# Kernel optimization log

Measured on AMD Instinct MI355X. Metric: run time of the kernel, lower is better.

The kernel has to match this reference:

```python
import jax, jax.numpy as jnp
import numpy as np
import math

N_HEAD = 16
K_SPARSE = 64

def setup_inputs() -> dict:
    key = jax.random.key(0)
    ks = jax.random.split(key, 12)
    B, T, C = 1, 2048, 1024
    s = 0.02
    return {
        "x":   jax.random.normal(ks[0], (B, T, C), jnp.float32),
        "Wq":  jax.random.normal(ks[1], (C, C), jnp.float32) * s,
        "bq":  jax.random.normal(ks[2], (C,), jnp.float32) * s,
        "Wk":  jax.random.normal(ks[3], (C, C), jnp.float32) * s,
        "bk":  jax.random.normal(ks[4], (C,), jnp.float32) * s,
        "Wv":  jax.random.normal(ks[5], (C, C), jnp.float32) * s,
        "bv":  jax.random.normal(ks[6], (C,), jnp.float32) * s,
        "Wo":  jax.random.normal(ks[7], (C, C), jnp.float32) * s,
        "bo":  jax.random.normal(ks[8], (C,), jnp.float32) * s,
        "Wks": jax.random.normal(ks[9], (C,), jnp.float32) * s,
        "bks": jax.random.normal(ks[10], (), jnp.float32) * s,
    }

def reference(x, Wq, bq, Wk, bk, Wv, bv, Wo, bo, Wks, bks):
    B, T, C = x.shape
    nh = N_HEAD
    hs = C // nh
    k_val = min(K_SPARSE, T)

    # projections -> (B, nh, T, hs)   (torch Linear: x @ W.T + b)
    q = (x @ Wq.T + bq).reshape(B, T, nh, hs).transpose(0, 2, 1, 3)
    k = (x @ Wk.T + bk).reshape(B, T, nh, hs).transpose(0, 2, 1, 3)
    v = (x @ Wv.T + bv).reshape(B, T, nh, hs).transpose(0, 2, 1, 3)

    # key scorer: per-token scalar score (B, T)
    key_scores = x @ Wks + bks

    # causal masking of scores, then per-query top-k key selection
    pos = jnp.arange(T)
    causal = pos[None, :] <= pos[:, None]                      # (T, T), True where key<=query
    masked = jnp.where(causal[None], key_scores[:, None, :], -jnp.inf)  # (B, T, T)
    _, top_k_idx = jax.lax.top_k(masked, k_val)                # (B, T, k)
    top_k_idx = jnp.minimum(top_k_idx, pos[None, :, None])     # clamp to <= query pos

    # gather sparse keys/values: (B, nh, T, k, hs)
    bi = jnp.arange(B)[:, None, None, None]
    hi = jnp.arange(nh)[None, :, None, None]
    gi = top_k_idx[:, None, :, :]                              # (B, 1, T, k)
    sparse_k = k[bi, hi, gi]                                   # (B, nh, T, k, hs)
    sparse_v = v[bi, hi, gi]

    scale = 1.0 / math.sqrt(hs)
    logits = jnp.einsum('bhtd,bhtkd->bhtk', q, sparse_k) * scale
    probs = jax.nn.softmax(logits, axis=-1)
    out = jnp.einsum('bhtk,bhtkd->bhtd', probs, sparse_v)      # (B, nh, T, hs)
    out = out.transpose(0, 2, 1, 3).reshape(B, T, C)
    return out @ Wo.T + bo
```

## Files before the change

### kernel.cpp

```cpp
#include <hip/hip_runtime.h>
#include <hip/hip_bf16.h>
#include <cstdint>
#include <cstddef>

#define T_DIM 2048
#define C_DIM 1024
#define NH 16
#define HS 64
#define KSP 64

#define GBM 128
#define GBN 64
#define GBK 128
#define OBM 64
#define OBN 64

#define ATB 32
#define USLOT 96
#define KSTR 72

typedef short short8 __attribute__((ext_vector_type(8)));
typedef float f32x4 __attribute__((ext_vector_type(4)));
typedef _Float16 half2_t __attribute__((ext_vector_type(2)));

__device__ __forceinline__ float bfu2f(unsigned short u) {
  unsigned v = ((unsigned)u) << 16;
  return __builtin_bit_cast(float, v);
}
__device__ __forceinline__ unsigned short f2bfu(float f) {
  unsigned u = __builtin_bit_cast(unsigned, f);
  unsigned r = (u + 0x7fffu + ((u >> 16) & 1u)) >> 16;
  return (unsigned short)r;
}
__device__ __forceinline__ unsigned short f2h(float f) {
  _Float16 h = (_Float16)f;
  return __builtin_bit_cast(unsigned short, h);
}
__device__ __forceinline__ float bflo(unsigned u) {
  return __builtin_bit_cast(float, u << 16);
}
__device__ __forceinline__ float bfhi(unsigned u) {
  return __builtin_bit_cast(float, u & 0xffff0000u);
}

__device__ __forceinline__ float dot2h(unsigned kbits, unsigned qbits, float acc) {
#if __has_builtin(__builtin_amdgcn_fdot2)
  return __builtin_amdgcn_fdot2(__builtin_bit_cast(half2_t, kbits),
                                __builtin_bit_cast(half2_t, qbits), acc, false);
#else
  half2_t kk = __builtin_bit_cast(half2_t, kbits);
  half2_t qq = __builtin_bit_cast(half2_t, qbits);
  return acc + (float)kk.x * (float)qq.x + (float)kk.y * (float)qq.y;
#endif
}

#define GLOAD_LDS16(gp, lp)                                                  \
  __builtin_amdgcn_global_load_lds(                                          \
      (const __attribute__((address_space(1))) void*)(gp),                   \
      (__attribute__((address_space(3))) void*)(lp), 16, 0, 0)

#define NSCORE (T_DIM / 4)
#define NCONV ((T_DIM * C_DIM + 4 * C_DIM * C_DIM) / 4 / 256)
__global__ __launch_bounds__(256) void convert_scores_kernel(
    const float* __restrict__ x, const float* __restrict__ Wq,
    const float* __restrict__ Wk, const float* __restrict__ Wv,
    const float* __restrict__ Wo, const float* __restrict__ Wks,
    const float* __restrict__ bks,
    unsigned short* __restrict__ xb, unsigned short* __restrict__ Wqb,
    unsigned short* __restrict__ Wkb, unsigned short* __restrict__ Wvb,
    unsigned short* __restrict__ Wob, float* __restrict__ scores) {
  if (blockIdx.x < NSCORE) {
    const int t = blockIdx.x * 4 + (threadIdx.x >> 6);
    const int lane = threadIdx.x & 63;
    const float* xrow = x + (size_t)t * C_DIM;
    float acc = 0.f;
    #pragma unroll 4
    for (int i = lane; i < C_DIM; i += 64)
      acc += xrow[i] * Wks[i];
    #pragma unroll
    for (int o = 32; o; o >>= 1) acc += __shfl_xor(acc, o);
    if (lane == 0) scores[t] = acc + bks[0];
    return;
  }
  const int i = (blockIdx.x - NSCORE) * 256 + threadIdx.x;
  const int NX4 = T_DIM * C_DIM / 4;
  const int NW4 = C_DIM * C_DIM / 4;
  const float* src;
  unsigned short* dst;
  int j = i;
  if (j < NX4) { src = x; dst = xb; }
  else {
    j -= NX4;
    int w = j / NW4;
    j -= w * NW4;
    src = (w == 0) ? Wq : (w == 1) ? Wk : (w == 2) ? Wv : Wo;
    dst = (w == 0) ? Wqb : (w == 1) ? Wkb : (w == 2) ? Wvb : Wob;
  }
  float4 f = reinterpret_cast<const float4*>(src)[j];
  ushort4 o;
  o.x = f2bfu(f.x); o.y = f2bfu(f.y); o.z = f2bfu(f.z); o.w = f2bfu(f.w);
  reinterpret_cast<ushort4*>(dst)[j] = o;
}

__device__ __forceinline__ void gemm_body_128x64(
    const unsigned short* __restrict__ A, const unsigned short* __restrict__ W,
    f32x4 acc[4][2], int bm, int bn, int tid,
    unsigned short* As, unsigned short* Ws) {
  const int w = tid >> 6, lane = tid & 63;
  const int quad = lane >> 4, r = lane & 15;
  const int wm = (w >> 1) * 64, wn = (w & 1) * 32;
  const int sub = lane >> 4;
  const int c = lane & 15;
  const unsigned short* Arow[8];
  const unsigned short* Wrow[4];
  #pragma unroll
  for (int i = 0; i < 8; ++i) {
    const int row = w * 32 + i * 4 + sub;
    Arow[i] = A + (size_t)(bm * GBM + row) * C_DIM + ((c ^ (row & 7)) * 8);
  }
  #pragma unroll
  for (int i = 0; i < 4; ++i) {
    const int row = w * 16 + i * 4 + sub;
    Wrow[i] = W + (size_t)(bn * GBN + row) * C_DIM + ((c ^ (row & 7)) * 8);
  }
  for (int kb = 0; kb < C_DIM; kb += GBK) {
    #pragma unroll
    for (int i = 0; i < 8; ++i)
      GLOAD_LDS16(Arow[i] + kb, &As[(w * 32 + i * 4) * GBK]);
    #pragma unroll
    for (int i = 0; i < 4; ++i)
      GLOAD_LDS16(Wrow[i] + kb, &Ws[(w * 16 + i * 4) * GBK]);
    __syncthreads();
    #pragma unroll
    for (int ks = 0; ks < 4; ++ks) {
      const int pc = ((ks * 4 + quad) ^ (r & 7)) * 8;
      short8 af[4], bfr[2];
      #pragma unroll
      for (int mi = 0; mi < 4; ++mi)
        af[mi] = *reinterpret_cast<const short8*>(&As[(wm + mi * 16 + r) * GBK + pc]);
      #pragma unroll
      for (int ni = 0; ni < 2; ++ni)
        bfr[ni] = *reinterpret_cast<const short8*>(&Ws[(wn + ni * 16 + r) * GBK + pc]);
      #pragma unroll
      for (int mi = 0; mi < 4; ++mi)
        #pragma unroll
        for (int ni = 0; ni < 2; ++ni)
          acc[mi][ni] = __builtin_amdgcn_mfma_f32_16x16x32_bf16(af[mi], bfr[ni], acc[mi][ni], 0, 0, 0);
    }
    __syncthreads();
  }
}

#define NRANK (T_DIM / 4)
__global__ __launch_bounds__(256) void gemm_qkv_rank_kernel(
    const unsigned short* __restrict__ A,
    const unsigned short* __restrict__ Wq, const unsigned short* __restrict__ Wk,
    const unsigned short* __restrict__ Wv,
    const float* __restrict__ bq, const float* __restrict__ bk,
    const float* __restrict__ bv,
    unsigned short* __restrict__ qo, unsigned short* __restrict__ ko,
    unsigned short* __restrict__ vo,
    const float* __restrict__ scores, int* __restrict__ sorted_idx) {
  __shared__ unsigned short lds[(GBM + GBN) * GBK];
  const int tid = threadIdx.x;
  if (blockIdx.x < NRANK) {
    float* ss = reinterpret_cast<float*>(lds);
    for (int j = tid; j < T_DIM; j += 256) ss[j] = scores[j];
    __syncthreads();
    const int w = tid >> 6, lane = tid & 63;
    const int i = blockIdx.x * 4 + w;
    const float si = ss[i];
    int rank = 0;
    #pragma unroll
    for (int step = 0; step < T_DIM / 64; ++step) {
      const int j = step * 64 + lane;
      const float sj = ss[j];
      rank += (int)((sj > si) || (sj == si && j < i));
    }
    #pragma unroll
    for (int o = 32; o; o >>= 1) rank += __shfl_xor(rank, o);
    if (lane == 0) sorted_idx[rank] = i;
    return;
  }
  const int bid = blockIdx.x - NRANK;
  const int per = (T_DIM / GBM) * (C_DIM / GBN);
  const int which = bid / per;
  const int rem = bid % per;
  const int bm = rem / (C_DIM / GBN);
  const int bn = rem % (C_DIM / GBN);
  const unsigned short* W = (which == 0) ? Wq : (which == 1) ? Wk : Wv;
  const float* bias = (which == 0) ? bq : (which == 1) ? bk : bv;
  unsigned short* out = (which == 0) ? qo : (which == 1) ? ko : vo;
  f32x4 acc[4][2] = {};
  gemm_body_128x64(A, W, acc, bm, bn, tid, lds, lds + GBM * GBK);
  const int w = tid >> 6, lane = tid & 63;
  const int quad = lane >> 4, r = lane & 15;
  const int wm = (w >> 1) * 64, wn = (w & 1) * 32;
  #pragma unroll
  for (int mi = 0; mi < 4; ++mi) {
    #pragma unroll
    for (int ni = 0; ni < 2; ++ni) {
      const int col = bn * GBN + wn + ni * 16 + r;
      const float bf = bias[col];
      #pragma unroll
      for (int i = 0; i < 4; ++i) {
        const int row = bm * GBM + wm + mi * 16 + quad * 4 + i;
        const float val = acc[mi][ni][i] + bf;
        out[(size_t)row * C_DIM + col] = (which == 2) ? f2bfu(val) : f2h(val);
      }
    }
  }
}

__device__ __forceinline__ void gemm_body_64x64(
    const unsigned short* __restrict__ A, const unsigned short* __restrict__ W,
    f32x4 acc[2][2], int bm, int bn, int tid) {
  __shared__ unsigned short As[OBM * GBK];
  __shared__ unsigned short Ws[OBN * GBK];
  const int w = tid >> 6, lane = tid & 63;
  const int quad = lane >> 4, r = lane & 15;
  const int wm = (w >> 1) * 32, wn = (w & 1) * 32;
  const int sub = lane >> 4;
  const int c = lane & 15;
  const unsigned short* Arow[4];
  const unsigned short* Wrow[4];
  #pragma unroll
  for (int i = 0; i < 4; ++i) {
    const int row = w * 16 + i * 4 + sub;
    Arow[i] = A + (size_t)(bm * OBM + row) * C_DIM + ((c ^ (row & 7)) * 8);
    Wrow[i] = W + (size_t)(bn * OBN + row) * C_DIM + ((c ^ (row & 7)) * 8);
  }
  for (int kb = 0; kb < C_DIM; kb += GBK) {
    #pragma unroll
    for (int i = 0; i < 4; ++i)
      GLOAD_LDS16(Arow[i] + kb, &As[(w * 16 + i * 4) * GBK]);
    #pragma unroll
    for (int i = 0; i < 4; ++i)
      GLOAD_LDS16(Wrow[i] + kb, &Ws[(w * 16 + i * 4) * GBK]);
    __syncthreads();
    #pragma unroll
    for (int ks = 0; ks < 4; ++ks) {
      const int pc = ((ks * 4 + quad) ^ (r & 7)) * 8;
      short8 af[2], bfr[2];
      #pragma unroll
      for (int mi = 0; mi < 2; ++mi)
        af[mi] = *reinterpret_cast<const short8*>(&As[(wm + mi * 16 + r) * GBK + pc]);
      #pragma unroll
      for (int ni = 0; ni < 2; ++ni)
        bfr[ni] = *reinterpret_cast<const short8*>(&Ws[(wn + ni * 16 + r) * GBK + pc]);
      #pragma unroll
      for (int mi = 0; mi < 2; ++mi)
        #pragma unroll
        for (int ni = 0; ni < 2; ++ni)
          acc[mi][ni] = __builtin_amdgcn_mfma_f32_16x16x32_bf16(af[mi], bfr[ni], acc[mi][ni], 0, 0, 0);
    }
    __syncthreads();
  }
}

__global__ __launch_bounds__(256) void gemm_o_f32_kernel(
    const unsigned short* __restrict__ A, const unsigned short* __restrict__ W,
    const float* __restrict__ bias, float* __restrict__ out) {
  const int tid = threadIdx.x;
  const int bm = blockIdx.x / (C_DIM / OBN);
  const int bn = blockIdx.x % (C_DIM / OBN);
  f32x4 acc[2][2] = {};
  gemm_body_64x64(A, W, acc, bm, bn, tid);
  const int w = tid >> 6, lane = tid & 63;
  const int quad = lane >> 4, r = lane & 15;
  const int wm = (w >> 1) * 32, wn = (w & 1) * 32;
  #pragma unroll
  for (int mi = 0; mi < 2; ++mi) {
    #pragma unroll
    for (int ni = 0; ni < 2; ++ni) {
      const int col = bn * OBN + wn + ni * 16 + r;
      const float bf = bias[col];
      #pragma unroll
      for (int i = 0; i < 4; ++i) {
        const int row = bm * OBM + wm + mi * 16 + quad * 4 + i;
        out[(size_t)row * C_DIM + col] = acc[mi][ni][i] + bf;
      }
    }
  }
}

__global__ __launch_bounds__(256) void select_kernel(
    const int* __restrict__ sorted_idx, int* __restrict__ sel) {
  const int tid = threadIdx.x;
  const int w = tid >> 6, lane = tid & 63;
  const int t = blockIdx.x * 4 + w;
  int* dst = sel + (size_t)t * KSP;
  if (t <= 63) {
    dst[lane] = (lane < t) ? lane : t;
    return;
  }
  const unsigned long long lt_mask = (1ull << lane) - 1ull;
  int count = 0;
  for (int chunk = 0; chunk < T_DIM / 64 && count < KSP; ++chunk) {
    int s = sorted_idx[chunk * 64 + lane];
    s = (s < 0) ? 0 : (s > T_DIM - 1 ? T_DIM - 1 : s);
    const bool ok = (s <= t);
    const unsigned long long mm = __ballot(ok);
    const int pos = count + __popcll(mm & lt_mask);
    if (ok && pos < KSP) dst[pos] = s;
    count += __popcll(mm);
  }
}

__global__ __launch_bounds__(256) void attn_kernel(
    const unsigned short* __restrict__ q, const unsigned short* __restrict__ k,
    const unsigned short* __restrict__ v, const int* __restrict__ sel,
    unsigned short* __restrict__ attn_out) {
  __shared__ unsigned short Kl[USLOT * KSTR];
  __shared__ unsigned short Vl[USLOT * KSTR];
  __shared__ short map_s[T_DIM];
  __shared__ short slots_tab[ATB][KSP];
  __shared__ short urows[USLOT];
  __shared__ int Ucnt;
  const int tb = blockIdx.x >> 4;
  const int h = blockIdx.x & (NH - 1);
  const int t0 = tb * ATB;
  const int tid = threadIdx.x;
  const int w = tid >> 6, lane = tid & 63;
  #pragma unroll
  for (int i = 0; i < T_DIM / 256; ++i) map_s[tid + i * 256] = -1;
  __syncthreads();
  int rowreg[ATB * KSP / 256];
  #pragma unroll
  for (int i = 0; i < ATB * KSP / 256; ++i) {
    rowreg[i] = sel[(size_t)t0 * KSP + tid + i * 256];
    map_s[rowreg[i]] = 1;
  }
  __syncthreads();
  if (w == 0) {
    const unsigned long long lt_mask = (1ull << lane) - 1ull;
    int count = 0;
    const int nch = (t0 + ATB + 63) >> 6;
    for (int c = 0; c < nch; ++c) {
      const int rowi = c * 64 + lane;
      const bool ok = (map_s[rowi] == 1);
      const unsigned long long mm = __ballot(ok);
      const int pos = count + __popcll(mm & lt_mask);
      if (ok) { map_s[rowi] = (short)pos; urows[pos] = (short)rowi; }
      count += __popcll(mm);
    }
    if (lane == 0) Ucnt = count;
  }
  __syncthreads();
  #pragma unroll
  for (int i = 0; i < ATB * KSP / 256; ++i)
    (&slots_tab[0][0])[tid + i * 256] = map_s[rowreg[i]];
  {
    const int U = Ucnt;
    const int e8 = tid & 7;
    for (int s = tid >> 3; s < U; s += 32) {
      const int row = urows[s];
      const size_t gb = (size_t)row * C_DIM + h * HS + e8 * 8;
      *reinterpret_cast<uint4*>(&Kl[s * KSTR + e8 * 8]) =
          *reinterpret_cast<const uint4*>(k + gb);
      *reinterpret_cast<uint4*>(&Vl[s * KSTR + e8 * 8]) =
          *reinterpret_cast<const uint4*>(v + gb);
    }
  }
  __syncthreads();
  const int c8 = lane & 7;
  const int ksub = lane >> 3;
  for (int i = 0; i < ATB / 4; ++i) {
    const int tt = w * (ATB / 4) + i;
    const int t = t0 + tt;
    const uint4 qraw =
        *reinterpret_cast<const uint4*>(q + (size_t)t * C_DIM + h * HS + 8 * c8);
    int slot[8];
    #pragma unroll
    for (int jj = 0; jj < 8; ++jj) slot[jj] = slots_tab[tt][8 * jj + ksub];
    float l[8];
    #pragma unroll
    for (int jj = 0; jj < 8; ++jj) {
      const uint4 raw =
          *reinterpret_cast<const uint4*>(&Kl[slot[jj] * KSTR + 8 * c8]);
      float pl = dot2h(raw.x, qraw.x, 0.f);
      pl = dot2h(raw.y, qraw.y, pl);
      pl = dot2h(raw.z, qraw.z, pl);
      pl = dot2h(raw.w, qraw.w, pl);
      pl *= 0.125f;
      pl += __shfl_xor(pl, 1);
      pl += __shfl_xor(pl, 2);
      pl += __shfl_xor(pl, 4);
      l[jj] = pl;
    }
    float m = l[0];
    #pragma unroll
    for (int jj = 1; jj < 8; ++jj) m = fmaxf(m, l[jj]);
    m = fmaxf(m, __shfl_xor(m, 8));
    m = fmaxf(m, __shfl_xor(m, 16));
    m = fmaxf(m, __shfl_xor(m, 32));
    float sum = 0.f;
    #pragma unroll
    for (int jj = 0; jj < 8; ++jj) {
      l[jj] = __expf(l[jj] - m);
      sum += l[jj];
    }
    sum += __shfl_xor(sum, 8);
    sum += __shfl_xor(sum, 16);
    sum += __shfl_xor(sum, 32);
    const float rs = 1.0f / sum;
    float a[8] = {0.f, 0.f, 0.f, 0.f, 0.f, 0.f, 0.f, 0.f};
    #pragma unroll
    for (int jj = 0; jj < 8; ++jj) {
      const uint4 raw =
          *reinterpret_cast<const uint4*>(&Vl[slot[jj] * KSTR + 8 * c8]);
      const float p = l[jj] * rs;
      a[0] += p * bflo(raw.x); a[1] += p * bfhi(raw.x);
      a[2] += p * bflo(raw.y); a[3] += p * bfhi(raw.y);
      a[4] += p * bflo(raw.z); a[5] += p * bfhi(raw.z);
      a[6] += p * bflo(raw.w); a[7] += p * bfhi(raw.w);
    }
    #pragma unroll
    for (int o = 8; o <= 32; o <<= 1) {
      #pragma unroll
      for (int z = 0; z < 8; ++z) a[z] += __shfl_xor(a[z], o);
    }
    if (ksub == 0) {
      ushort4 o0, o1;
      o0.x = f2bfu(a[0]); o0.y = f2bfu(a[1]); o0.z = f2bfu(a[2]); o0.w = f2bfu(a[3]);
      o1.x = f2bfu(a[4]); o1.y = f2bfu(a[5]); o1.z = f2bfu(a[6]); o1.w = f2bfu(a[7]);
      ushort4* dst =
          reinterpret_cast<ushort4*>(attn_out + (size_t)t * C_DIM + h * HS + 8 * c8);
      dst[0] = o0;
      dst[1] = o1;
    }
  }
}

extern "C" void kernel_launch(void* const* d_in, const int* in_sizes, int n_in,
                              void* d_out, int out_size, void* d_ws, size_t ws_size,
                              hipStream_t stream) {
  const float* x   = (const float*)d_in[0];
  const float* Wq  = (const float*)d_in[1];
  const float* bq  = (const float*)d_in[2];
  const float* Wk  = (const float*)d_in[3];
  const float* bk  = (const float*)d_in[4];
  const float* Wv  = (const float*)d_in[5];
  const float* bv  = (const float*)d_in[6];
  const float* Wo  = (const float*)d_in[7];
  const float* bo  = (const float*)d_in[8];
  const float* Wks = (const float*)d_in[9];
  const float* bks = (const float*)d_in[10];
  float* out = (float*)d_out;

  char* ws = (char*)d_ws;
  size_t off = 0;
  float* scores = (float*)(ws + off); off += 8192;
  int*   sorted = (int*)(ws + off);   off += 8192;
  int*   sel    = (int*)(ws + off);   off += (size_t)T_DIM * KSP * 4;
  unsigned short* xb  = (unsigned short*)(ws + off); off += (size_t)T_DIM * C_DIM * 2;
  unsigned short* Wqb = (unsigned short*)(ws + off); off += (size_t)C_DIM * C_DIM * 2;
  unsigned short* Wkb = (unsigned short*)(ws + off); off += (size_t)C_DIM * C_DIM * 2;
  unsigned short* Wvb = (unsigned short*)(ws + off); off += (size_t)C_DIM * C_DIM * 2;
  unsigned short* Wob = (unsigned short*)(ws + off); off += (size_t)C_DIM * C_DIM * 2;
  unsigned short* qb  = (unsigned short*)(ws + off); off += (size_t)T_DIM * C_DIM * 2;
  unsigned short* kb  = (unsigned short*)(ws + off); off += (size_t)T_DIM * C_DIM * 2;
  unsigned short* vb  = (unsigned short*)(ws + off); off += (size_t)T_DIM * C_DIM * 2;
  unsigned short* ab  = xb;

  convert_scores_kernel<<<NSCORE + NCONV, 256, 0, stream>>>(
      x, Wq, Wk, Wv, Wo, Wks, bks, xb, Wqb, Wkb, Wvb, Wob, scores);

  gemm_qkv_rank_kernel<<<NRANK + 3 * (T_DIM / GBM) * (C_DIM / GBN), 256, 0,
                         stream>>>(
      xb, Wqb, Wkb, Wvb, bq, bk, bv, qb, kb, vb, scores, sorted);

  select_kernel<<<T_DIM / 4, 256, 0, stream>>>(sorted, sel);

  attn_kernel<<<(T_DIM / ATB) * NH, 256, 0, stream>>>(qb, kb, vb, sel, ab);

  gemm_o_f32_kernel<<<(T_DIM / OBM) * (C_DIM / OBN), 256, 0, stream>>>(
      ab, Wob, bo, out);
}
```

Before: 170.8 us.

## Fuse top-k selection into attention and build per-block union from first query

New measurement: 160.9 us. 5.8% less time.

```diff
diff --git a/kernel.cpp b/kernel.cpp
--- a/kernel.cpp
+++ b/kernel.cpp
@@ -15,18 +15,14 @@
 #define OBM 64
 #define OBN 64
 
-#define ATB 32
-#define USLOT 96
-#define KSTR 72
+#define ATB 16
+#define USLOT (KSP + ATB - 1)
+#define KSTR 66
 
 typedef short short8 __attribute__((ext_vector_type(8)));
 typedef float f32x4 __attribute__((ext_vector_type(4)));
 typedef _Float16 half2_t __attribute__((ext_vector_type(2)));
 
-__device__ __forceinline__ float bfu2f(unsigned short u) {
-  unsigned v = ((unsigned)u) << 16;
-  return __builtin_bit_cast(float, v);
-}
 __device__ __forceinline__ unsigned short f2bfu(float f) {
   unsigned u = __builtin_bit_cast(unsigned, f);
   unsigned r = (u + 0x7fffu + ((u >> 16) & 1u)) >> 16;
@@ -284,76 +280,60 @@
   }
 }
 
-__global__ __launch_bounds__(256) void select_kernel(
-    const int* __restrict__ sorted_idx, int* __restrict__ sel) {
-  const int tid = threadIdx.x;
-  const int w = tid >> 6, lane = tid & 63;
-  const int t = blockIdx.x * 4 + w;
-  int* dst = sel + (size_t)t * KSP;
-  if (t <= 63) {
-    dst[lane] = (lane < t) ? lane : t;
-    return;
-  }
-  const unsigned long long lt_mask = (1ull << lane) - 1ull;
-  int count = 0;
-  for (int chunk = 0; chunk < T_DIM / 64 && count < KSP; ++chunk) {
-    int s = sorted_idx[chunk * 64 + lane];
-    s = (s < 0) ? 0 : (s > T_DIM - 1 ? T_DIM - 1 : s);
-    const bool ok = (s <= t);
-    const unsigned long long mm = __ballot(ok);
-    const int pos = count + __popcll(mm & lt_mask);
-    if (ok && pos < KSP) dst[pos] = s;
-    count += __popcll(mm);
-  }
-}
-
 __global__ __launch_bounds__(256) void attn_kernel(
     const unsigned short* __restrict__ q, const unsigned short* __restrict__ k,
-    const unsigned short* __restrict__ v, const int* __restrict__ sel,
+    const unsigned short* __restrict__ v, const int* __restrict__ sorted_idx,
     unsigned short* __restrict__ attn_out) {
   __shared__ unsigned short Kl[USLOT * KSTR];
   __shared__ unsigned short Vl[USLOT * KSTR];
   __shared__ short map_s[T_DIM];
-  __shared__ short slots_tab[ATB][KSP];
+  __shared__ short rows_tab[ATB][KSP];
   __shared__ short urows[USLOT];
-  __shared__ int Ucnt;
   const int tb = blockIdx.x >> 4;
   const int h = blockIdx.x & (NH - 1);
   const int t0 = tb * ATB;
   const int tid = threadIdx.x;
   const int w = tid >> 6, lane = tid & 63;
-  #pragma unroll
-  for (int i = 0; i < T_DIM / 256; ++i) map_s[tid + i * 256] = -1;
+  const int c8 = lane & 7;
+  const int ksub = lane >> 3;
+  uint4 qr[ATB / 4];
+  #pragma unroll
+  for (int li = 0; li < ATB / 4; ++li) {
+    const int t = t0 + w * (ATB / 4) + li;
+    qr[li] = *reinterpret_cast<const uint4*>(q + (size_t)t * C_DIM + h * HS + 8 * c8);
+  }
+  const unsigned long long lt_mask = (1ull << lane) - 1ull;
+  for (int li = 0; li < ATB / 4; ++li) {
+    const int tt = w * (ATB / 4) + li;
+    const int t = t0 + tt;
+    if (t <= 63) {
+      rows_tab[tt][lane] = (short)((lane < t) ? lane : t);
+    } else {
+      int count = 0;
+      for (int c = 0; c < T_DIM / 64 && count < KSP; ++c) {
+        int s = sorted_idx[c * 64 + lane];
+        s = (s < 0) ? 0 : (s > T_DIM - 1 ? T_DIM - 1 : s);
+        const bool ok = (s <= t);
+        const unsigned long long mm = __ballot(ok);
+        const int pos = count + __popcll(mm & lt_mask);
+        if (ok && pos < KSP) rows_tab[tt][pos] = (short)s;
+        count += __popcll(mm);
+      }
+    }
+    if (w == 0 && li == 0) {
+      const int r0 = rows_tab[0][lane];
+      map_s[r0] = (short)lane;
+      urows[lane] = (short)r0;
+      if (lane < ATB - 1) {
+        map_s[t0 + 1 + lane] = (short)(KSP + lane);
+        urows[KSP + lane] = (short)(t0 + 1 + lane);
+      }
+    }
+  }
   __syncthreads();
-  int rowreg[ATB * KSP / 256];
-  #pragma unroll
-  for (int i = 0; i < ATB * KSP / 256; ++i) {
-    rowreg[i] = sel[(size_t)t0 * KSP + tid + i * 256];
-    map_s[rowreg[i]] = 1;
-  }
-  __syncthreads();
-  if (w == 0) {
-    const unsigned long long lt_mask = (1ull << lane) - 1ull;
-    int count = 0;
-    const int nch = (t0 + ATB + 63) >> 6;
-    for (int c = 0; c < nch; ++c) {
-      const int rowi = c * 64 + lane;
-      const bool ok = (map_s[rowi] == 1);
-      const unsigned long long mm = __ballot(ok);
-      const int pos = count + __popcll(mm & lt_mask);
-      if (ok) { map_s[rowi] = (short)pos; urows[pos] = (short)rowi; }
-      count += __popcll(mm);
-    }
-    if (lane == 0) Ucnt = count;
-  }
-  __syncthreads();
-  #pragma unroll
-  for (int i = 0; i < ATB * KSP / 256; ++i)
-    (&slots_tab[0][0])[tid + i * 256] = map_s[rowreg[i]];
   {
-    const int U = Ucnt;
     const int e8 = tid & 7;
-    for (int s = tid >> 3; s < U; s += 32) {
+    for (int s = tid >> 3; s < USLOT; s += 32) {
       const int row = urows[s];
       const size_t gb = (size_t)row * C_DIM + h * HS + e8 * 8;
       *reinterpret_cast<uint4*>(&Kl[s * KSTR + e8 * 8]) =
@@ -363,16 +343,14 @@
     }
   }
   __syncthreads();
-  const int c8 = lane & 7;
-  const int ksub = lane >> 3;
-  for (int i = 0; i < ATB / 4; ++i) {
-    const int tt = w * (ATB / 4) + i;
+  for (int li = 0; li < ATB / 4; ++li) {
+    const int tt = w * (ATB / 4) + li;
     const int t = t0 + tt;
-    const uint4 qraw =
-        *reinterpret_cast<const uint4*>(q + (size_t)t * C_DIM + h * HS + 8 * c8);
+    const uint4 qraw = qr[li];
     int slot[8];
     #pragma unroll
-    for (int jj = 0; jj < 8; ++jj) slot[jj] = slots_tab[tt][8 * jj + ksub];
+    for (int jj = 0; jj < 8; ++jj)
+      slot[jj] = map_s[rows_tab[tt][8 * jj + ksub]];
     float l[8];
     #pragma unroll
     for (int jj = 0; jj < 8; ++jj) {
@@ -452,7 +430,6 @@
   size_t off = 0;
   float* scores = (float*)(ws + off); off += 8192;
   int*   sorted = (int*)(ws + off);   off += 8192;
-  int*   sel    = (int*)(ws + off);   off += (size_t)T_DIM * KSP * 4;
   unsigned short* xb  = (unsigned short*)(ws + off); off += (size_t)T_DIM * C_DIM * 2;
   unsigned short* Wqb = (unsigned short*)(ws + off); off += (size_t)C_DIM * C_DIM * 2;
   unsigned short* Wkb = (unsigned short*)(ws + off); off += (size_t)C_DIM * C_DIM * 2;
@@ -470,9 +447,7 @@
                          stream>>>(
       xb, Wqb, Wkb, Wvb, bq, bk, bv, qb, kb, vb, scores, sorted);
 
-  select_kernel<<<T_DIM / 4, 256, 0, stream>>>(sorted, sel);
-
-  attn_kernel<<<(T_DIM / ATB) * NH, 256, 0, stream>>>(qb, kb, vb, sel, ab);
+  attn_kernel<<<(T_DIM / ATB) * NH, 256, 0, stream>>>(qb, kb, vb, sorted, ab);
 
   gemm_o_f32_kernel<<<(T_DIM / OBM) * (C_DIM / OBN), 256, 0, stream>>>(
       ab, Wob, bo, out);
```
